# Kernel tuning notes

Hardware: AMD Instinct MI355X
Metric: run time of the kernel (lower is better)

The kernel has to match this reference:

```python
import jax, jax.numpy as jnp
import numpy as np

B, T, D = 64, 8192, 128

def setup_inputs() -> dict:
    key = jax.random.key(0)
    ks = jax.random.split(key, 6)
    H_r = jax.random.normal(ks[0], (B, T, D), dtype=jnp.float32)
    mask_r = jax.random.randint(ks[1], (B, T), 0, 2, dtype=jnp.int32)
    h_tm1 = jax.random.normal(ks[2], (B, D), dtype=jnp.float32)
    # xavier-ish scaling for linear weights
    s = 1.0 / np.sqrt(D)
    V_w = jax.random.normal(ks[3], (D, D), dtype=jnp.float32) * s
    Wa_w = jax.random.normal(ks[4], (D, D), dtype=jnp.float32) * s
    V_b = jnp.zeros((D,), dtype=jnp.float32)
    Wa_b = jnp.zeros((D,), dtype=jnp.float32)
    v = jax.random.normal(ks[5], (D,), dtype=jnp.float32) * 0.05
    c = jnp.ones((1,), dtype=jnp.float32)
    return {"H_r": H_r, "mask_r": mask_r, "h_tm1": h_tm1, "V_w": V_w,
            "V_b": V_b, "Wa_w": Wa_w, "Wa_b": Wa_b, "v": v, "c": c}

def masked_softmax(x, m, axis=-1):
    x = jnp.clip(x, -15.0, 15.0)
    x = x * m
    e_x = jnp.exp(x - jnp.max(x, axis=axis, keepdims=True))
    e_x = e_x * m
    return e_x / (jnp.sum(e_x, axis=axis, keepdims=True) + 1e-6)

def reference(H_r, mask_r, h_tm1, V_w, V_b, Wa_w, Wa_b, v, c):
    m = mask_r.astype(jnp.float32)                      # [B,T]
    Fk = jnp.einsum('btd,od->bto', H_r, V_w) + V_b      # [B,T,D]
    Fk_prime = h_tm1 @ Wa_w.T + Wa_b                    # [B,D]
    Fk = jnp.tanh(Fk + Fk_prime[:, None, :])
    beta = Fk @ v + c                                   # [B,T]
    beta = masked_softmax(beta, m, axis=-1)
    z = jnp.einsum('bt,btd->bd', beta, H_r)             # [B,D]
    return (z, beta)
```

## Files before the change

### kernel.cpp

```cpp
#include <hip/hip_runtime.h>
#include <math.h>

#define BB 64
#define TT 8192
#define DD 128
#define RPT 64
#define NT 16
#define RPBLK (RPT * NT)
#define NBLK (BB * TT / RPBLK)
#define BPB (TT / RPBLK)

typedef float f32x4 __attribute__((ext_vector_type(4)));
typedef __bf16 bf16x4 __attribute__((ext_vector_type(4)));
typedef __bf16 bf16x8 __attribute__((ext_vector_type(8)));

__device__ __forceinline__ float fast_tanh(float x) {
    float t = __expf(2.f * x);
    return 1.f - 2.f * __builtin_amdgcn_rcpf(t + 1.f);
}

__device__ __forceinline__ float bf_at_lo16(unsigned u) { return __uint_as_float(u << 16); }
__device__ __forceinline__ float bf_at_hi16(unsigned u) { return __uint_as_float(u & 0xffff0000u); }

__global__ __launch_bounds__(256) void prep_kernel(
    const float* __restrict__ Vw, const float* __restrict__ Waw,
    const float* __restrict__ Wab, const float* __restrict__ h_tm1,
    __bf16* __restrict__ Vw_bf, float* __restrict__ fkp) {
    const int b = blockIdx.x, tid = threadIdx.x;
    const int i = b * 256 + tid;
    const int r = i >> 7, cidx = i & 127;
    Vw_bf[r * DD + (cidx ^ ((r & 7) << 3))] = (__bf16)Vw[i];

    if (tid < DD) {
        const float* __restrict__ w = Waw + tid * DD;
        const float* __restrict__ h = h_tm1 + b * DD;
        float a0 = 0.f, a1 = 0.f, a2 = 0.f, a3 = 0.f;
#pragma unroll
        for (int d = 0; d < DD; d += 4) {
            float4 w4 = *reinterpret_cast<const float4*>(w + d);
            a0 = fmaf(w4.x, h[d + 0], a0);
            a1 = fmaf(w4.y, h[d + 1], a1);
            a2 = fmaf(w4.z, h[d + 2], a2);
            a3 = fmaf(w4.w, h[d + 3], a3);
        }
        fkp[b * DD + tid] = (a0 + a1) + (a2 + a3) + Wab[tid];
    }
}

__global__ __launch_bounds__(256, 2) void beta_z_kernel(
    const float* __restrict__ H, const __bf16* __restrict__ Vw_bf,
    const float* __restrict__ Vb, const float* __restrict__ fkp,
    const float* __restrict__ vvec, const float* __restrict__ cptr,
    const int* __restrict__ mask,
    float* __restrict__ eout,
    float* __restrict__ zpart) {
    const int tid  = threadIdx.x;
    const int wv   = tid >> 6;
    const int lane = tid & 63;
    const int cl   = lane & 15;
    const int kg   = lane >> 4;
    const int base_row = blockIdx.x * RPBLK;
    const int b    = base_row >> 13;

    __shared__ __align__(16) char s_vw[DD * DD * 2];
    __shared__ __align__(16) char s_h[2][RPT * DD * 2];
    __shared__ float s_z[4][DD];

    {
        const char* __restrict__ wg = (const char*)Vw_bf;
#pragma unroll
        for (int i = 0; i < 8; ++i) {
            __builtin_amdgcn_global_load_lds(
                (const void*)(wg + wv * 8192 + i * 1024 + lane * 16),
                (void*)(s_vw + wv * 8192 + i * 1024), 16, 0, 0);
        }
    }
    float4 hreg[8];
    {
        const float4* __restrict__ Hg =
            reinterpret_cast<const float4*>(H + (size_t)base_row * DD);
#pragma unroll
        for (int i = 0; i < 8; ++i) hreg[i] = Hg[i * 256 + tid];
#pragma unroll
        for (int i = 0; i < 8; ++i) {
            bf16x4 r;
            r[0] = (__bf16)hreg[i].x; r[1] = (__bf16)hreg[i].y;
            r[2] = (__bf16)hreg[i].z; r[3] = (__bf16)hreg[i].w;
            const int off = (i * 256 + tid) * 8;
            const int row = off >> 8;
            *reinterpret_cast<bf16x4*>(s_h[0] + (off ^ ((row & 7) << 4))) = r;
        }
    }
    __syncthreads();

    const float cval = cptr[0];
    float biasv[8], vvv[8];
#pragma unroll
    for (int nt = 0; nt < 8; ++nt) {
        const int col = nt * 16 + cl;
        biasv[nt] = Vb[col] + fkp[b * DD + col];
        vvv[nt]   = vvec[col];
    }

    const int ra   = wv * 16 + cl;
    const int swzA = (cl & 7) << 4;
    f32x4 zlo[4], zhi[4];
#pragma unroll
    for (int kk = 0; kk < 4; ++kk) {
        zlo[kk] = (f32x4){0.f, 0.f, 0.f, 0.f};
        zhi[kk] = (f32x4){0.f, 0.f, 0.f, 0.f};
    }

    for (int t = 0; t < NT; ++t) {
        const int cur    = t & 1;
        const int grow0  = base_row + t * RPT;
        const int myrow0 = grow0 + wv * 16;

        if (t + 1 < NT) {
            const float4* __restrict__ Hn =
                reinterpret_cast<const float4*>(H + (size_t)(grow0 + RPT) * DD);
#pragma unroll
            for (int i = 0; i < 8; ++i) hreg[i] = Hn[i * 256 + tid];
        }
        const float mfl = (float)mask[myrow0 + cl];

        uint4  au[4];
        bf16x8 af[4];
#pragma unroll
        for (int kk = 0; kk < 4; ++kk) {
            const int abyte = ra * 256 + kk * 64 + kg * 16;
            au[kk] = *reinterpret_cast<const uint4*>(s_h[cur] + (abyte ^ swzA));
            af[kk] = __builtin_bit_cast(bf16x8, au[kk]);
        }

        f32x4 acc[8];
#pragma unroll
        for (int nt = 0; nt < 8; ++nt) acc[nt] = (f32x4){0.f, 0.f, 0.f, 0.f};
#pragma unroll
        for (int kk = 0; kk < 4; ++kk) {
#pragma unroll
            for (int nt = 0; nt < 8; ++nt) {
                const int rb    = nt * 16 + cl;
                const int bbyte = (rb * 256 + kk * 64 + kg * 16) ^ ((rb & 7) << 4);
                bf16x8 bfr = *reinterpret_cast<const bf16x8*>(s_vw + bbyte);
                acc[nt] = __builtin_amdgcn_mfma_f32_16x16x32_bf16(af[kk], bfr, acc[nt], 0, 0, 0);
            }
        }

        float part[4] = {0.f, 0.f, 0.f, 0.f};
#pragma unroll
        for (int nt = 0; nt < 8; ++nt) {
#pragma unroll
            for (int j = 0; j < 4; ++j)
                part[j] = fmaf(fast_tanh(acc[nt][j] + biasv[nt]), vvv[nt], part[j]);
        }
#pragma unroll
        for (int off = 1; off < 16; off <<= 1) {
#pragma unroll
            for (int j = 0; j < 4; ++j) part[j] += __shfl_xor(part[j], off);
        }
        float epj[4];
#pragma unroll
        for (int j = 0; j < 4; ++j) {
            const float mv = __shfl(mfl, kg * 4 + j);
            const float x  = fminf(fmaxf(cval + part[j], -15.f), 15.f);
            epj[j] = __expf(x * mv - 15.f) * mv;
        }
        if (cl == 0) {
#pragma unroll
            for (int j = 0; j < 4; ++j) eout[myrow0 + kg * 4 + j] = epj[j];
        }

        const float er0 = __shfl(epj[0], (cl >> 2) << 4);
        const float er1 = __shfl(epj[1], (cl >> 2) << 4);
        const float er2 = __shfl(epj[2], (cl >> 2) << 4);
        const float er3 = __shfl(epj[3], (cl >> 2) << 4);
        const int sel = cl & 3;
        const float e_cl = sel == 0 ? er0 : (sel == 1 ? er1 : (sel == 2 ? er2 : er3));
#pragma unroll
        for (int kk = 0; kk < 4; ++kk) {
            zlo[kk][0] = fmaf(e_cl, bf_at_lo16(au[kk].x), zlo[kk][0]);
            zlo[kk][1] = fmaf(e_cl, bf_at_hi16(au[kk].x), zlo[kk][1]);
            zlo[kk][2] = fmaf(e_cl, bf_at_lo16(au[kk].y), zlo[kk][2]);
            zlo[kk][3] = fmaf(e_cl, bf_at_hi16(au[kk].y), zlo[kk][3]);
            zhi[kk][0] = fmaf(e_cl, bf_at_lo16(au[kk].z), zhi[kk][0]);
            zhi[kk][1] = fmaf(e_cl, bf_at_hi16(au[kk].z), zhi[kk][1]);
            zhi[kk][2] = fmaf(e_cl, bf_at_lo16(au[kk].w), zhi[kk][2]);
            zhi[kk][3] = fmaf(e_cl, bf_at_hi16(au[kk].w), zhi[kk][3]);
        }

        if (t + 1 < NT) {
#pragma unroll
            for (int i = 0; i < 8; ++i) {
                bf16x4 r;
                r[0] = (__bf16)hreg[i].x; r[1] = (__bf16)hreg[i].y;
                r[2] = (__bf16)hreg[i].z; r[3] = (__bf16)hreg[i].w;
                const int off = (i * 256 + tid) * 8;
                const int row = off >> 8;
                *reinterpret_cast<bf16x4*>(s_h[cur ^ 1] + (off ^ ((row & 7) << 4))) = r;
            }
        }
        __syncthreads();
    }

#pragma unroll
    for (int off = 1; off < 16; off <<= 1) {
#pragma unroll
        for (int kk = 0; kk < 4; ++kk) {
#pragma unroll
            for (int j = 0; j < 4; ++j) {
                zlo[kk][j] += __shfl_xor(zlo[kk][j], off);
                zhi[kk][j] += __shfl_xor(zhi[kk][j], off);
            }
        }
    }
    if (cl == 0) {
#pragma unroll
        for (int kk = 0; kk < 4; ++kk) {
#pragma unroll
            for (int j = 0; j < 4; ++j) {
                s_z[wv][kk * 32 + kg * 8 + j]     = zlo[kk][j];
                s_z[wv][kk * 32 + kg * 8 + 4 + j] = zhi[kk][j];
            }
        }
    }
    __syncthreads();
    if (tid < DD) {
        zpart[(size_t)blockIdx.x * DD + tid] =
            (s_z[0][tid] + s_z[1][tid]) + (s_z[2][tid] + s_z[3][tid]);
    }
}

__global__ __launch_bounds__(256) void denom_z_kernel(
    float* __restrict__ eout, const int* __restrict__ mask,
    const float* __restrict__ zpart, float* __restrict__ out_z) {
    const int b = blockIdx.x, tid = threadIdx.x;
    float* __restrict__ e = eout + (size_t)b * TT;
    const int* __restrict__ mrow = mask + (size_t)b * TT;
    __shared__ float sE[256], sM[256];
    __shared__ int sA[256];

    float E = 0.f, M = 0.f;
    int any0 = 0;
    for (int t = tid; t < TT; t += 256) {
        float ep = e[t];
        E += ep;
        M = fmaxf(M, ep);
        any0 |= (mrow[t] == 0);
    }
    sE[tid] = E; sM[tid] = M; sA[tid] = any0;
    __syncthreads();
    for (int s = 128; s > 0; s >>= 1) {
        if (tid < s) {
            sE[tid] += sE[tid + s];
            sM[tid] = fmaxf(sM[tid], sM[tid + s]);
            sA[tid] |= sA[tid + s];
        }
        __syncthreads();
    }
    const float scale = sA[0] ? fmaxf(sM[0], 3.0590232e-7f ) : sM[0];
    const float dn = sE[0] + 1e-6f * scale;
    const float inv = 1.f / dn;

    for (int t = tid; t < TT; t += 256) e[t] *= inv;

    if (tid < DD) {
        const float* __restrict__ zp = zpart + (size_t)b * BPB * DD + tid;
        float s = 0.f;
#pragma unroll
        for (int cc = 0; cc < BPB; ++cc) s += zp[cc * DD];
        out_z[b * DD + tid] = s * inv;
    }
}

extern "C" void kernel_launch(void* const* d_in, const int* in_sizes, int n_in,
                              void* d_out, int out_size, void* d_ws, size_t ws_size,
                              hipStream_t stream) {
    const float* H     = (const float*)d_in[0];
    const int*   mask  = (const int*)d_in[1];
    const float* h_tm1 = (const float*)d_in[2];
    const float* V_w   = (const float*)d_in[3];
    const float* V_b   = (const float*)d_in[4];
    const float* Wa_w  = (const float*)d_in[5];
    const float* Wa_b  = (const float*)d_in[6];
    const float* v     = (const float*)d_in[7];
    const float* c     = (const float*)d_in[8];

    float* out_z    = (float*)d_out;
    float* out_beta = (float*)d_out + BB * DD;

    float* ws     = (float*)d_ws;
    float* fkp    = ws;
    float* zpart  = fkp + BB * DD;
    __bf16* Vw_bf = (__bf16*)(zpart + NBLK * DD);

    prep_kernel<<<BB, 256, 0, stream>>>(V_w, Wa_w, Wa_b, h_tm1, Vw_bf, fkp);
    beta_z_kernel<<<NBLK, 256, 0, stream>>>(H, Vw_bf, V_b, fkp, v, c, mask,
                                            out_beta, zpart);
    denom_z_kernel<<<BB, 256, 0, stream>>>(out_beta, mask, zpart, out_z);
}
```

Before: 81.04 us.

## Stream fp32 H tiles directly into LDS per wave and drop block barriers

Each wave now loads its own 16 rows of H as fp32 straight into a swizzled shared-memory region with global_load_lds. The rows are converted to bf16 only when the MFMA fragments are built, and the z accumulation reads the fp32 values directly. This removes the register staging, the bf16 pack-and-store pass and the per-iteration __syncthreads, leaving a per-wave vmcnt wait. The risks are a single-buffered tile that is overwritten soon after the LDS reads and a doubled LDS read footprint per row.

```diff
diff --git a/kernel.cpp b/kernel.cpp
--- a/kernel.cpp
+++ b/kernel.cpp
@@ -11,7 +11,6 @@
 #define BPB (TT / RPBLK)
 
 typedef float f32x4 __attribute__((ext_vector_type(4)));
-typedef __bf16 bf16x4 __attribute__((ext_vector_type(4)));
 typedef __bf16 bf16x8 __attribute__((ext_vector_type(8)));
 
 __device__ __forceinline__ float fast_tanh(float x) {
@@ -19,8 +18,12 @@
     return 1.f - 2.f * __builtin_amdgcn_rcpf(t + 1.f);
 }
 
-__device__ __forceinline__ float bf_at_lo16(unsigned u) { return __uint_as_float(u << 16); }
-__device__ __forceinline__ float bf_at_hi16(unsigned u) { return __uint_as_float(u & 0xffff0000u); }
+__device__ __forceinline__ bf16x8 cvt8(f32x4 a, f32x4 b) {
+    bf16x8 r;
+    r[0] = (__bf16)a[0]; r[1] = (__bf16)a[1]; r[2] = (__bf16)a[2]; r[3] = (__bf16)a[3];
+    r[4] = (__bf16)b[0]; r[5] = (__bf16)b[1]; r[6] = (__bf16)b[2]; r[7] = (__bf16)b[3];
+    return r;
+}
 
 __global__ __launch_bounds__(256) void prep_kernel(
     const float* __restrict__ Vw, const float* __restrict__ Waw,
@@ -63,7 +66,7 @@
     const int b    = base_row >> 13;
 
     __shared__ __align__(16) char s_vw[DD * DD * 2];
-    __shared__ __align__(16) char s_h[2][RPT * DD * 2];
+    __shared__ __align__(16) char s_hf[RPT * DD * 4];
     __shared__ float s_z[4][DD];
 
     {
@@ -74,23 +77,18 @@
                 (const void*)(wg + wv * 8192 + i * 1024 + lane * 16),
                 (void*)(s_vw + wv * 8192 + i * 1024), 16, 0, 0);
         }
-    }
-    float4 hreg[8];
-    {
-        const float4* __restrict__ Hg =
-            reinterpret_cast<const float4*>(H + (size_t)base_row * DD);
-#pragma unroll
-        for (int i = 0; i < 8; ++i) hreg[i] = Hg[i * 256 + tid];
+        const char* __restrict__ hb =
+            (const char*)H + (size_t)(base_row + wv * 16) * 512;
 #pragma unroll
         for (int i = 0; i < 8; ++i) {
-            bf16x4 r;
-            r[0] = (__bf16)hreg[i].x; r[1] = (__bf16)hreg[i].y;
-            r[2] = (__bf16)hreg[i].z; r[3] = (__bf16)hreg[i].w;
-            const int off = (i * 256 + tid) * 8;
-            const int row = off >> 8;
-            *reinterpret_cast<bf16x4*>(s_h[0] + (off ^ ((row & 7) << 4))) = r;
-        }
-    }
+            const int off = i * 1024 + lane * 16;
+            const int r16 = off >> 9;
+            __builtin_amdgcn_global_load_lds(
+                (const void*)(hb + (off ^ ((r16 & 7) << 4))),
+                (void*)(s_hf + wv * 8192 + i * 1024), 16, 0, 0);
+        }
+    }
+    float mcur = (float)mask[base_row + wv * 16 + cl];
     __syncthreads();
 
     const float cval = cptr[0];
@@ -102,7 +100,6 @@
         vvv[nt]   = vvec[col];
     }
 
-    const int ra   = wv * 16 + cl;
     const int swzA = (cl & 7) << 4;
     f32x4 zlo[4], zhi[4];
 #pragma unroll
@@ -112,25 +109,33 @@
     }
 
     for (int t = 0; t < NT; ++t) {
-        const int cur    = t & 1;
-        const int grow0  = base_row + t * RPT;
-        const int myrow0 = grow0 + wv * 16;
-
+        const int myrow0 = base_row + t * RPT + wv * 16;
+
+        asm volatile("s_waitcnt vmcnt(0)" ::: "memory");
+
+        f32x4 alo[4], ahi[4];
+        bf16x8 af[4];
+#pragma unroll
+        for (int kk = 0; kk < 4; ++kk) {
+            const int abyte = (wv * 16 + cl) * 512 + kk * 128 + kg * 32;
+            alo[kk] = *reinterpret_cast<const f32x4*>(s_hf + ((abyte)      ^ swzA));
+            ahi[kk] = *reinterpret_cast<const f32x4*>(s_hf + ((abyte + 16) ^ swzA));
+            af[kk]  = cvt8(alo[kk], ahi[kk]);
+        }
+
+        float mnext = 0.f;
         if (t + 1 < NT) {
-            const float4* __restrict__ Hn =
-                reinterpret_cast<const float4*>(H + (size_t)(grow0 + RPT) * DD);
-#pragma unroll
-            for (int i = 0; i < 8; ++i) hreg[i] = Hn[i * 256 + tid];
-        }
-        const float mfl = (float)mask[myrow0 + cl];
-
-        uint4  au[4];
-        bf16x8 af[4];
-#pragma unroll
-        for (int kk = 0; kk < 4; ++kk) {
-            const int abyte = ra * 256 + kk * 64 + kg * 16;
-            au[kk] = *reinterpret_cast<const uint4*>(s_h[cur] + (abyte ^ swzA));
-            af[kk] = __builtin_bit_cast(bf16x8, au[kk]);
+            const char* __restrict__ hb =
+                (const char*)H + (size_t)(myrow0 + RPT) * 512;
+#pragma unroll
+            for (int i = 0; i < 8; ++i) {
+                const int off = i * 1024 + lane * 16;
+                const int r16 = off >> 9;
+                __builtin_amdgcn_global_load_lds(
+                    (const void*)(hb + (off ^ ((r16 & 7) << 4))),
+                    (void*)(s_hf + wv * 8192 + i * 1024), 16, 0, 0);
+            }
+            mnext = (float)mask[myrow0 + RPT + cl];
         }
 
         f32x4 acc[8];
@@ -162,7 +167,7 @@
         float epj[4];
 #pragma unroll
         for (int j = 0; j < 4; ++j) {
-            const float mv = __shfl(mfl, kg * 4 + j);
+            const float mv = __shfl(mcur, kg * 4 + j);
             const float x  = fminf(fmaxf(cval + part[j], -15.f), 15.f);
             epj[j] = __expf(x * mv - 15.f) * mv;
         }
@@ -179,28 +184,14 @@
         const float e_cl = sel == 0 ? er0 : (sel == 1 ? er1 : (sel == 2 ? er2 : er3));
 #pragma unroll
         for (int kk = 0; kk < 4; ++kk) {
-            zlo[kk][0] = fmaf(e_cl, bf_at_lo16(au[kk].x), zlo[kk][0]);
-            zlo[kk][1] = fmaf(e_cl, bf_at_hi16(au[kk].x), zlo[kk][1]);
-            zlo[kk][2] = fmaf(e_cl, bf_at_lo16(au[kk].y), zlo[kk][2]);
-            zlo[kk][3] = fmaf(e_cl, bf_at_hi16(au[kk].y), zlo[kk][3]);
-            zhi[kk][0] = fmaf(e_cl, bf_at_lo16(au[kk].z), zhi[kk][0]);
-            zhi[kk][1] = fmaf(e_cl, bf_at_hi16(au[kk].z), zhi[kk][1]);
-            zhi[kk][2] = fmaf(e_cl, bf_at_lo16(au[kk].w), zhi[kk][2]);
-            zhi[kk][3] = fmaf(e_cl, bf_at_hi16(au[kk].w), zhi[kk][3]);
-        }
-
-        if (t + 1 < NT) {
-#pragma unroll
-            for (int i = 0; i < 8; ++i) {
-                bf16x4 r;
-                r[0] = (__bf16)hreg[i].x; r[1] = (__bf16)hreg[i].y;
-                r[2] = (__bf16)hreg[i].z; r[3] = (__bf16)hreg[i].w;
-                const int off = (i * 256 + tid) * 8;
-                const int row = off >> 8;
-                *reinterpret_cast<bf16x4*>(s_h[cur ^ 1] + (off ^ ((row & 7) << 4))) = r;
-            }
-        }
-        __syncthreads();
+#pragma unroll
+            for (int j = 0; j < 4; ++j) {
+                zlo[kk][j] = fmaf(e_cl, alo[kk][j], zlo[kk][j]);
+                zhi[kk][j] = fmaf(e_cl, ahi[kk][j], zhi[kk][j]);
+            }
+        }
+
+        mcur = mnext;
     }
 
 #pragma unroll
```

Measured after the change: 86.87 us. 7.2% more time.

## Split GEMM columns across wave pairs with 512-thread blocks

Applied to the files above, without the earlier changes.

Doubles the block to 8 waves, where each pair of waves shares a 16-row tile and each wave computes half of the 128 output columns. Partial dot products with v are combined through a small shared buffer, and only one wave of each pair accumulates z. The aim is more waves in flight and lower per-wave register pressure, to hide H load latency. In exchange it adds an extra block-wide barrier per tile and leaves half the waves idle during the z accumulation.

```diff
diff --git a/kernel.cpp b/kernel.cpp
--- a/kernel.cpp
+++ b/kernel.cpp
@@ -47,7 +47,7 @@
     }
 }
 
-__global__ __launch_bounds__(256, 2) void beta_z_kernel(
+__global__ __launch_bounds__(512, 4) void beta_z_kernel(
     const float* __restrict__ H, const __bf16* __restrict__ Vw_bf,
     const float* __restrict__ Vb, const float* __restrict__ fkp,
     const float* __restrict__ vvec, const float* __restrict__ cptr,
@@ -59,34 +59,38 @@
     const int lane = tid & 63;
     const int cl   = lane & 15;
     const int kg   = lane >> 4;
+    const int pair = wv >> 1;
+    const int half = wv & 1;
     const int base_row = blockIdx.x * RPBLK;
     const int b    = base_row >> 13;
 
     __shared__ __align__(16) char s_vw[DD * DD * 2];
     __shared__ __align__(16) char s_h[2][RPT * DD * 2];
     __shared__ float s_z[4][DD];
+    __shared__ float s_pp[4][2][16];
 
     {
         const char* __restrict__ wg = (const char*)Vw_bf;
 #pragma unroll
-        for (int i = 0; i < 8; ++i) {
+        for (int i = 0; i < 4; ++i) {
+            const int c = wv * 4 + i;
             __builtin_amdgcn_global_load_lds(
-                (const void*)(wg + wv * 8192 + i * 1024 + lane * 16),
-                (void*)(s_vw + wv * 8192 + i * 1024), 16, 0, 0);
-        }
-    }
-    float4 hreg[8];
+                (const void*)(wg + c * 1024 + lane * 16),
+                (void*)(s_vw + c * 1024), 16, 0, 0);
+        }
+    }
+    float4 hreg[4];
     {
         const float4* __restrict__ Hg =
             reinterpret_cast<const float4*>(H + (size_t)base_row * DD);
 #pragma unroll
-        for (int i = 0; i < 8; ++i) hreg[i] = Hg[i * 256 + tid];
-#pragma unroll
-        for (int i = 0; i < 8; ++i) {
+        for (int i = 0; i < 4; ++i) hreg[i] = Hg[i * 512 + tid];
+#pragma unroll
+        for (int i = 0; i < 4; ++i) {
             bf16x4 r;
             r[0] = (__bf16)hreg[i].x; r[1] = (__bf16)hreg[i].y;
             r[2] = (__bf16)hreg[i].z; r[3] = (__bf16)hreg[i].w;
-            const int off = (i * 256 + tid) * 8;
+            const int off = (i * 512 + tid) * 8;
             const int row = off >> 8;
             *reinterpret_cast<bf16x4*>(s_h[0] + (off ^ ((row & 7) << 4))) = r;
         }
@@ -94,15 +98,15 @@
     __syncthreads();
 
     const float cval = cptr[0];
-    float biasv[8], vvv[8];
-#pragma unroll
-    for (int nt = 0; nt < 8; ++nt) {
-        const int col = nt * 16 + cl;
-        biasv[nt] = Vb[col] + fkp[b * DD + col];
-        vvv[nt]   = vvec[col];
-    }
-
-    const int ra   = wv * 16 + cl;
+    float biasv[4], vvv[4];
+#pragma unroll
+    for (int n = 0; n < 4; ++n) {
+        const int col = (half * 4 + n) * 16 + cl;
+        biasv[n] = Vb[col] + fkp[b * DD + col];
+        vvv[n]   = vvec[col];
+    }
+
+    const int ra   = pair * 16 + cl;
     const int swzA = (cl & 7) << 4;
     f32x4 zlo[4], zhi[4];
 #pragma unroll
@@ -114,13 +118,13 @@
     for (int t = 0; t < NT; ++t) {
         const int cur    = t & 1;
         const int grow0  = base_row + t * RPT;
-        const int myrow0 = grow0 + wv * 16;
+        const int myrow0 = grow0 + pair * 16;
 
         if (t + 1 < NT) {
             const float4* __restrict__ Hn =
                 reinterpret_cast<const float4*>(H + (size_t)(grow0 + RPT) * DD);
 #pragma unroll
-            for (int i = 0; i < 8; ++i) hreg[i] = Hn[i * 256 + tid];
+            for (int i = 0; i < 4; ++i) hreg[i] = Hn[i * 512 + tid];
         }
         const float mfl = (float)mask[myrow0 + cl];
 
@@ -133,69 +137,78 @@
             af[kk] = __builtin_bit_cast(bf16x8, au[kk]);
         }
 
-        f32x4 acc[8];
-#pragma unroll
-        for (int nt = 0; nt < 8; ++nt) acc[nt] = (f32x4){0.f, 0.f, 0.f, 0.f};
+        f32x4 acc[4];
+#pragma unroll
+        for (int n = 0; n < 4; ++n) acc[n] = (f32x4){0.f, 0.f, 0.f, 0.f};
 #pragma unroll
         for (int kk = 0; kk < 4; ++kk) {
 #pragma unroll
-            for (int nt = 0; nt < 8; ++nt) {
-                const int rb    = nt * 16 + cl;
+            for (int n = 0; n < 4; ++n) {
+                const int rb    = (half * 4 + n) * 16 + cl;
                 const int bbyte = (rb * 256 + kk * 64 + kg * 16) ^ ((rb & 7) << 4);
                 bf16x8 bfr = *reinterpret_cast<const bf16x8*>(s_vw + bbyte);
-                acc[nt] = __builtin_amdgcn_mfma_f32_16x16x32_bf16(af[kk], bfr, acc[nt], 0, 0, 0);
+                acc[n] = __builtin_amdgcn_mfma_f32_16x16x32_bf16(af[kk], bfr, acc[n], 0, 0, 0);
             }
         }
 
         float part[4] = {0.f, 0.f, 0.f, 0.f};
 #pragma unroll
-        for (int nt = 0; nt < 8; ++nt) {
+        for (int n = 0; n < 4; ++n) {
 #pragma unroll
             for (int j = 0; j < 4; ++j)
-                part[j] = fmaf(fast_tanh(acc[nt][j] + biasv[nt]), vvv[nt], part[j]);
+                part[j] = fmaf(fast_tanh(acc[n][j] + biasv[n]), vvv[n], part[j]);
         }
 #pragma unroll
         for (int off = 1; off < 16; off <<= 1) {
 #pragma unroll
             for (int j = 0; j < 4; ++j) part[j] += __shfl_xor(part[j], off);
         }
+        if (cl == 0) {
+#pragma unroll
+            for (int j = 0; j < 4; ++j) s_pp[pair][half][kg * 4 + j] = part[j];
+        }
+        __syncthreads();
+
         float epj[4];
 #pragma unroll
         for (int j = 0; j < 4; ++j) {
+            const float ptot = s_pp[pair][0][kg * 4 + j] + s_pp[pair][1][kg * 4 + j];
             const float mv = __shfl(mfl, kg * 4 + j);
-            const float x  = fminf(fmaxf(cval + part[j], -15.f), 15.f);
+            const float x  = fminf(fmaxf(cval + ptot, -15.f), 15.f);
             epj[j] = __expf(x * mv - 15.f) * mv;
         }
-        if (cl == 0) {
+        if (half == 0 && cl == 0) {
 #pragma unroll
             for (int j = 0; j < 4; ++j) eout[myrow0 + kg * 4 + j] = epj[j];
         }
 
-        const float er0 = __shfl(epj[0], (cl >> 2) << 4);
-        const float er1 = __shfl(epj[1], (cl >> 2) << 4);
-        const float er2 = __shfl(epj[2], (cl >> 2) << 4);
-        const float er3 = __shfl(epj[3], (cl >> 2) << 4);
-        const int sel = cl & 3;
-        const float e_cl = sel == 0 ? er0 : (sel == 1 ? er1 : (sel == 2 ? er2 : er3));
-#pragma unroll
-        for (int kk = 0; kk < 4; ++kk) {
-            zlo[kk][0] = fmaf(e_cl, bf_at_lo16(au[kk].x), zlo[kk][0]);
-            zlo[kk][1] = fmaf(e_cl, bf_at_hi16(au[kk].x), zlo[kk][1]);
-            zlo[kk][2] = fmaf(e_cl, bf_at_lo16(au[kk].y), zlo[kk][2]);
-            zlo[kk][3] = fmaf(e_cl, bf_at_hi16(au[kk].y), zlo[kk][3]);
-            zhi[kk][0] = fmaf(e_cl, bf_at_lo16(au[kk].z), zhi[kk][0]);
-            zhi[kk][1] = fmaf(e_cl, bf_at_hi16(au[kk].z), zhi[kk][1]);
-            zhi[kk][2] = fmaf(e_cl, bf_at_lo16(au[kk].w), zhi[kk][2]);
-            zhi[kk][3] = fmaf(e_cl, bf_at_hi16(au[kk].w), zhi[kk][3]);
+        if (half == 0) {
+            const float er0 = __shfl(epj[0], (cl >> 2) << 4);
+            const float er1 = __shfl(epj[1], (cl >> 2) << 4);
+            const float er2 = __shfl(epj[2], (cl >> 2) << 4);
+            const float er3 = __shfl(epj[3], (cl >> 2) << 4);
+            const int sel = cl & 3;
+            const float e_cl = sel == 0 ? er0 : (sel == 1 ? er1 : (sel == 2 ? er2 : er3));
+#pragma unroll
+            for (int kk = 0; kk < 4; ++kk) {
+                zlo[kk][0] = fmaf(e_cl, bf_at_lo16(au[kk].x), zlo[kk][0]);
+                zlo[kk][1] = fmaf(e_cl, bf_at_hi16(au[kk].x), zlo[kk][1]);
+                zlo[kk][2] = fmaf(e_cl, bf_at_lo16(au[kk].y), zlo[kk][2]);
+                zlo[kk][3] = fmaf(e_cl, bf_at_hi16(au[kk].y), zlo[kk][3]);
+                zhi[kk][0] = fmaf(e_cl, bf_at_lo16(au[kk].z), zhi[kk][0]);
+                zhi[kk][1] = fmaf(e_cl, bf_at_hi16(au[kk].z), zhi[kk][1]);
+                zhi[kk][2] = fmaf(e_cl, bf_at_lo16(au[kk].w), zhi[kk][2]);
+                zhi[kk][3] = fmaf(e_cl, bf_at_hi16(au[kk].w), zhi[kk][3]);
+            }
         }
 
         if (t + 1 < NT) {
 #pragma unroll
-            for (int i = 0; i < 8; ++i) {
+            for (int i = 0; i < 4; ++i) {
                 bf16x4 r;
                 r[0] = (__bf16)hreg[i].x; r[1] = (__bf16)hreg[i].y;
                 r[2] = (__bf16)hreg[i].z; r[3] = (__bf16)hreg[i].w;
-                const int off = (i * 256 + tid) * 8;
+                const int off = (i * 512 + tid) * 8;
                 const int row = off >> 8;
                 *reinterpret_cast<bf16x4*>(s_h[cur ^ 1] + (off ^ ((row & 7) << 4))) = r;
             }
@@ -214,13 +227,13 @@
             }
         }
     }
-    if (cl == 0) {
+    if (half == 0 && cl == 0) {
 #pragma unroll
         for (int kk = 0; kk < 4; ++kk) {
 #pragma unroll
             for (int j = 0; j < 4; ++j) {
-                s_z[wv][kk * 32 + kg * 8 + j]     = zlo[kk][j];
-                s_z[wv][kk * 32 + kg * 8 + 4 + j] = zhi[kk][j];
+                s_z[pair][kk * 32 + kg * 8 + j]     = zlo[kk][j];
+                s_z[pair][kk * 32 + kg * 8 + 4 + j] = zhi[kk][j];
             }
         }
     }
@@ -295,7 +308,7 @@
     __bf16* Vw_bf = (__bf16*)(zpart + NBLK * DD);
 
     prep_kernel<<<BB, 256, 0, stream>>>(V_w, Wa_w, Wa_b, h_tm1, Vw_bf, fkp);
-    beta_z_kernel<<<NBLK, 256, 0, stream>>>(H, Vw_bf, V_b, fkp, v, c, mask,
+    beta_z_kernel<<<NBLK, 512, 0, stream>>>(H, Vw_bf, V_b, fkp, v, c, mask,
                                             out_beta, zpart);
     denom_z_kernel<<<BB, 256, 0, stream>>>(out_beta, mask, zpart, out_z);
 }
```

Measured after the change: 135.6 us. 1.67x slower.

## Software-pipeline MFMA and tanh/softmax epilogue across consecutive tiles

Applied to the files above, without the earlier changes.

Restructures the main loop so that the tanh/exp epilogue and z accumulation of tile t-1 are interleaved with the MFMA matmul of tile t. Accumulators and A fragments are double-buffered in registers, the loop is unrolled by two, and a sched_barrier constrains instruction ordering. The goal is to overlap matrix-core work with the VALU/transcendental work. The cost is higher register pressure, which could lower occupancy or cause spills.

```diff
diff --git a/kernel.cpp b/kernel.cpp
--- a/kernel.cpp
+++ b/kernel.cpp
@@ -111,97 +111,114 @@
         zhi[kk] = (f32x4){0.f, 0.f, 0.f, 0.f};
     }
 
-    for (int t = 0; t < NT; ++t) {
-        const int cur    = t & 1;
-        const int grow0  = base_row + t * RPT;
-        const int myrow0 = grow0 + wv * 16;
-
-        if (t + 1 < NT) {
-            const float4* __restrict__ Hn =
-                reinterpret_cast<const float4*>(H + (size_t)(grow0 + RPT) * DD);
-#pragma unroll
-            for (int i = 0; i < 8; ++i) hreg[i] = Hn[i * 256 + tid];
-        }
-        const float mfl = (float)mask[myrow0 + cl];
-
-        uint4  au[4];
-        bf16x8 af[4];
-#pragma unroll
-        for (int kk = 0; kk < 4; ++kk) {
-            const int abyte = ra * 256 + kk * 64 + kg * 16;
-            au[kk] = *reinterpret_cast<const uint4*>(s_h[cur] + (abyte ^ swzA));
-            af[kk] = __builtin_bit_cast(bf16x8, au[kk]);
-        }
-
-        f32x4 acc[8];
-#pragma unroll
-        for (int nt = 0; nt < 8; ++nt) acc[nt] = (f32x4){0.f, 0.f, 0.f, 0.f};
-#pragma unroll
-        for (int kk = 0; kk < 4; ++kk) {
-#pragma unroll
-            for (int nt = 0; nt < 8; ++nt) {
-                const int rb    = nt * 16 + cl;
-                const int bbyte = (rb * 256 + kk * 64 + kg * 16) ^ ((rb & 7) << 4);
-                bf16x8 bfr = *reinterpret_cast<const bf16x8*>(s_vw + bbyte);
-                acc[nt] = __builtin_amdgcn_mfma_f32_16x16x32_bf16(af[kk], bfr, acc[nt], 0, 0, 0);
-            }
-        }
-
-        float part[4] = {0.f, 0.f, 0.f, 0.f};
-#pragma unroll
-        for (int nt = 0; nt < 8; ++nt) {
-#pragma unroll
-            for (int j = 0; j < 4; ++j)
-                part[j] = fmaf(fast_tanh(acc[nt][j] + biasv[nt]), vvv[nt], part[j]);
-        }
-#pragma unroll
-        for (int off = 1; off < 16; off <<= 1) {
-#pragma unroll
-            for (int j = 0; j < 4; ++j) part[j] += __shfl_xor(part[j], off);
-        }
-        float epj[4];
-#pragma unroll
-        for (int j = 0; j < 4; ++j) {
-            const float mv = __shfl(mfl, kg * 4 + j);
-            const float x  = fminf(fmaxf(cval + part[j], -15.f), 15.f);
-            epj[j] = __expf(x * mv - 15.f) * mv;
-        }
-        if (cl == 0) {
-#pragma unroll
-            for (int j = 0; j < 4; ++j) eout[myrow0 + kg * 4 + j] = epj[j];
-        }
-
-        const float er0 = __shfl(epj[0], (cl >> 2) << 4);
-        const float er1 = __shfl(epj[1], (cl >> 2) << 4);
-        const float er2 = __shfl(epj[2], (cl >> 2) << 4);
-        const float er3 = __shfl(epj[3], (cl >> 2) << 4);
-        const int sel = cl & 3;
-        const float e_cl = sel == 0 ? er0 : (sel == 1 ? er1 : (sel == 2 ? er2 : er3));
-#pragma unroll
-        for (int kk = 0; kk < 4; ++kk) {
-            zlo[kk][0] = fmaf(e_cl, bf_at_lo16(au[kk].x), zlo[kk][0]);
-            zlo[kk][1] = fmaf(e_cl, bf_at_hi16(au[kk].x), zlo[kk][1]);
-            zlo[kk][2] = fmaf(e_cl, bf_at_lo16(au[kk].y), zlo[kk][2]);
-            zlo[kk][3] = fmaf(e_cl, bf_at_hi16(au[kk].y), zlo[kk][3]);
-            zhi[kk][0] = fmaf(e_cl, bf_at_lo16(au[kk].z), zhi[kk][0]);
-            zhi[kk][1] = fmaf(e_cl, bf_at_hi16(au[kk].z), zhi[kk][1]);
-            zhi[kk][2] = fmaf(e_cl, bf_at_lo16(au[kk].w), zhi[kk][2]);
-            zhi[kk][3] = fmaf(e_cl, bf_at_hi16(au[kk].w), zhi[kk][3]);
-        }
-
-        if (t + 1 < NT) {
-#pragma unroll
-            for (int i = 0; i < 8; ++i) {
-                bf16x4 r;
-                r[0] = (__bf16)hreg[i].x; r[1] = (__bf16)hreg[i].y;
-                r[2] = (__bf16)hreg[i].z; r[3] = (__bf16)hreg[i].w;
-                const int off = (i * 256 + tid) * 8;
-                const int row = off >> 8;
-                *reinterpret_cast<bf16x4*>(s_h[cur ^ 1] + (off ^ ((row & 7) << 4))) = r;
-            }
-        }
-        __syncthreads();
-    }
+    f32x4 acc2[2][8];
+    uint4 au2[2][4];
+    float mfl2[2];
+
+#define EPILOGUE(S, MYROW0)                                                     \
+    {                                                                           \
+        float part[4] = {0.f, 0.f, 0.f, 0.f};                                   \
+        _Pragma("unroll")                                                       \
+        for (int nt = 0; nt < 8; ++nt) {                                        \
+            _Pragma("unroll")                                                   \
+            for (int j = 0; j < 4; ++j)                                         \
+                part[j] = fmaf(fast_tanh(acc2[S][nt][j] + biasv[nt]), vvv[nt],  \
+                               part[j]);                                        \
+        }                                                                       \
+        _Pragma("unroll")                                                       \
+        for (int off = 1; off < 16; off <<= 1) {                                \
+            _Pragma("unroll")                                                   \
+            for (int j = 0; j < 4; ++j) part[j] += __shfl_xor(part[j], off);    \
+        }                                                                       \
+        float epj[4];                                                           \
+        _Pragma("unroll")                                                       \
+        for (int j = 0; j < 4; ++j) {                                           \
+            const float mv = __shfl(mfl2[S], kg * 4 + j);                       \
+            const float x  = fminf(fmaxf(cval + part[j], -15.f), 15.f);         \
+            epj[j] = __expf(x * mv - 15.f) * mv;                                \
+        }                                                                       \
+        if (cl == 0) {                                                          \
+            _Pragma("unroll")                                                   \
+            for (int j = 0; j < 4; ++j) eout[(MYROW0) + kg * 4 + j] = epj[j];   \
+        }                                                                       \
+        const float er0 = __shfl(epj[0], (cl >> 2) << 4);                       \
+        const float er1 = __shfl(epj[1], (cl >> 2) << 4);                       \
+        const float er2 = __shfl(epj[2], (cl >> 2) << 4);                       \
+        const float er3 = __shfl(epj[3], (cl >> 2) << 4);                       \
+        const int sel = cl & 3;                                                 \
+        const float e_cl =                                                      \
+            sel == 0 ? er0 : (sel == 1 ? er1 : (sel == 2 ? er2 : er3));         \
+        _Pragma("unroll")                                                       \
+        for (int kk = 0; kk < 4; ++kk) {                                        \
+            zlo[kk][0] = fmaf(e_cl, bf_at_lo16(au2[S][kk].x), zlo[kk][0]);      \
+            zlo[kk][1] = fmaf(e_cl, bf_at_hi16(au2[S][kk].x), zlo[kk][1]);      \
+            zlo[kk][2] = fmaf(e_cl, bf_at_lo16(au2[S][kk].y), zlo[kk][2]);      \
+            zlo[kk][3] = fmaf(e_cl, bf_at_hi16(au2[S][kk].y), zlo[kk][3]);      \
+            zhi[kk][0] = fmaf(e_cl, bf_at_lo16(au2[S][kk].z), zhi[kk][0]);      \
+            zhi[kk][1] = fmaf(e_cl, bf_at_hi16(au2[S][kk].z), zhi[kk][1]);      \
+            zhi[kk][2] = fmaf(e_cl, bf_at_lo16(au2[S][kk].w), zhi[kk][2]);      \
+            zhi[kk][3] = fmaf(e_cl, bf_at_hi16(au2[S][kk].w), zhi[kk][3]);      \
+        }                                                                       \
+    }
+
+#define STEP(T, CUR, PRV)                                                       \
+    {                                                                           \
+        const int myrow0 = base_row + (T) * RPT + wv * 16;                      \
+        if ((T) + 1 < NT) {                                                     \
+            const float4* __restrict__ Hn = reinterpret_cast<const float4*>(    \
+                H + (size_t)(base_row + ((T) + 1) * RPT) * DD);                 \
+            _Pragma("unroll")                                                   \
+            for (int i = 0; i < 8; ++i) hreg[i] = Hn[i * 256 + tid];            \
+        }                                                                       \
+        mfl2[CUR] = (float)mask[myrow0 + cl];                                   \
+                 \
+        __builtin_amdgcn_sched_barrier(0x3CF);                                  \
+        if ((T) > 0) EPILOGUE(PRV, myrow0 - RPT)                                \
+        _Pragma("unroll")                                                       \
+        for (int kk = 0; kk < 4; ++kk) {                                        \
+            const int abyte = ra * 256 + kk * 64 + kg * 16;                     \
+            au2[CUR][kk] =                                                      \
+                *reinterpret_cast<const uint4*>(s_h[CUR] + (abyte ^ swzA));     \
+        }                                                                       \
+        _Pragma("unroll")                                                       \
+        for (int nt = 0; nt < 8; ++nt)                                          \
+            acc2[CUR][nt] = (f32x4){0.f, 0.f, 0.f, 0.f};                        \
+        _Pragma("unroll")                                                       \
+        for (int kk = 0; kk < 4; ++kk) {                                        \
+            const bf16x8 afk = __builtin_bit_cast(bf16x8, au2[CUR][kk]);        \
+            _Pragma("unroll")                                                   \
+            for (int nt = 0; nt < 8; ++nt) {                                    \
+                const int rb    = nt * 16 + cl;                                 \
+                const int bbyte =                                               \
+                    (rb * 256 + kk * 64 + kg * 16) ^ ((rb & 7) << 4);           \
+                bf16x8 bfr = *reinterpret_cast<const bf16x8*>(s_vw + bbyte);    \
+                acc2[CUR][nt] = __builtin_amdgcn_mfma_f32_16x16x32_bf16(        \
+                    afk, bfr, acc2[CUR][nt], 0, 0, 0);                          \
+            }                                                                   \
+        }                                                                       \
+        if ((T) + 1 < NT) {                                                     \
+            _Pragma("unroll")                                                   \
+            for (int i = 0; i < 8; ++i) {                                       \
+                bf16x4 r;                                                       \
+                r[0] = (__bf16)hreg[i].x; r[1] = (__bf16)hreg[i].y;             \
+                r[2] = (__bf16)hreg[i].z; r[3] = (__bf16)hreg[i].w;             \
+                const int off = (i * 256 + tid) * 8;                            \
+                const int row = off >> 8;                                       \
+                *reinterpret_cast<bf16x4*>(s_h[(CUR) ^ 1] +                     \
+                                           (off ^ ((row & 7) << 4))) = r;       \
+            }                                                                   \
+        }                                                                       \
+        __syncthreads();                                                        \
+    }
+
+    for (int tp = 0; tp < NT; tp += 2) {
+        STEP(tp, 0, 1)
+        STEP(tp + 1, 1, 0)
+    }
+    EPILOGUE(1, base_row + (NT - 1) * RPT + wv * 16)
+
+#undef STEP
+#undef EPILOGUE
 
 #pragma unroll
     for (int off = 1; off < 16; off <<= 1) {
```

Measured after the change: 82.14 us. About the same (+1.4%).
